# Kernel optimization log

Hardware: AMD Instinct MI355X
Metric: run time of the kernel (lower is better)

## Reference

```python
import jax, jax.numpy as jnp
import numpy as np

S, B, NC = 16, 8, 5
D, H, DH = 256, 16, 16
PS, IMG = 7, 28
P = (IMG // PS) ** 2  # 16 patches
L = 2
PD = PS * PS * 1  # 49
EF, EFT = 4, 0.5
DFT = int(EFT * D)


def layernorm(x, g, b, eps=1e-5):
    m = x.mean(-1, keepdims=True)
    v = ((x - m) ** 2).mean(-1, keepdims=True)
    return (x - m) / jnp.sqrt(v + eps) * g + b


def patchify(x):
    # 's b c (h p1) (w p2) -> s b (h w) (p1 p2 c)'
    s, bb, c, hh, ww = x.shape
    h, w = hh // PS, ww // PS
    x = x.reshape(s, bb, c, h, PS, w, PS)
    x = x.transpose(0, 1, 3, 5, 4, 6, 2)
    return x.reshape(s, bb, h * w, PS * PS * c)


def srwm(x, Wy, Wq, Wk, wb, ln_g, ln_b):
    # Stateful self-referential weight matrix layer (Irie et al. 2022).
    # x: (S, Bn, h*dh); Wy/Wq/Wk: (h, dh, dh); wb: (h, 4, dh)
    s, bn, dim = x.shape
    h, dh = Wy.shape[0], Wy.shape[1]
    xs = x.reshape(s, bn, h, dh)
    bc = lambda W: jnp.broadcast_to(W[None], (bn,) + W.shape)

    def step(carry, xt):
        Wy, Wq, Wk, wb = carry
        y = jnp.einsum('bhij,bhj->bhi', Wy, xt)
        q = jnp.einsum('bhij,bhj->bhi', Wq, xt)
        k = jnp.einsum('bhij,bhj->bhi', Wk, xt)
        beta = jax.nn.sigmoid(jnp.einsum('bhcj,bhj->bhc', wb, xt))  # (Bn,h,4)
        qs = jax.nn.softmax(q, -1)
        ks = jax.nn.softmax(k, -1)
        # old values retrieved with k, target values generated with q
        vy_k = jnp.einsum('bhij,bhj->bhi', Wy, ks)
        vq_k = jnp.einsum('bhij,bhj->bhi', Wq, ks)
        vk_k = jnp.einsum('bhij,bhj->bhi', Wk, ks)
        vb_k = jnp.einsum('bhcj,bhj->bhc', wb, ks)
        vy_q = jax.nn.softmax(jnp.einsum('bhij,bhj->bhi', Wy, qs), -1)
        vq_q = jnp.einsum('bhij,bhj->bhi', Wq, qs)
        vk_q = jnp.einsum('bhij,bhj->bhi', Wk, qs)
        vb_q = jnp.einsum('bhcj,bhj->bhc', wb, qs)
        upd = lambda d, bt: bt[..., None, None] * d[..., None] * ks[..., None, :]
        Wy = Wy + upd(vy_q - vy_k, beta[..., 0])
        Wq = Wq + upd(vq_q - vq_k, beta[..., 1])
        Wk = Wk + upd(vk_q - vk_k, beta[..., 2])
        wb = wb + beta[..., 3, None, None] * (vb_q - vb_k)[..., None] * ks[..., None, :]
        return (Wy, Wq, Wk, wb), y

    _, ys = jax.lax.scan(step, (bc(Wy), bc(Wq), bc(Wk), bc(wb)), xs)
    return layernorm(ys.reshape(s, bn, dim), ln_g, ln_b)


def setup_inputs():
    key = jax.random.key(0)
    ks = iter(jax.random.split(key, 64))
    n = lambda shape, sc: jax.random.normal(next(ks), shape, jnp.float32) * sc
    return dict(
        x=jax.random.normal(next(ks), (S, B, 1, IMG, IMG), jnp.float32),
        fb=jax.random.randint(next(ks), (S, B), 0, NC),
        in_W=n((PD + NC, D), (PD + NC) ** -0.5), in_b=jnp.zeros((D,)),
        tk_Wy=n((L, 1, P, P), P ** -0.5), tk_Wq=n((L, 1, P, P), 0.01 * P ** -0.5),
        tk_Wk=n((L, 1, P, P), P ** -0.5), tk_wb=n((L, 1, 4, P), P ** -0.5),
        tk_lng=jnp.ones((L, P)), tk_lnb=jnp.zeros((L, P)),
        tkm_g=jnp.ones((L, D)), tkm_b=jnp.zeros((L, D)),
        tkm_W1=n((L, P, EF * P), P ** -0.5), tkm_b1=jnp.zeros((L, EF * P)),
        tkm_W2=n((L, EF * P, P), (EF * P) ** -0.5), tkm_b2=jnp.zeros((L, P)),
        ch_Wy=n((L, H, DH, DH), DH ** -0.5), ch_Wq=n((L, H, DH, DH), 0.01 * DH ** -0.5),
        ch_Wk=n((L, H, DH, DH), DH ** -0.5), ch_wb=n((L, H, 4, DH), DH ** -0.5),
        ch_lng=jnp.ones((L, D)), ch_lnb=jnp.zeros((L, D)),
        chm_g=jnp.ones((L, D)), chm_b=jnp.zeros((L, D)),
        chm_W1=n((L, D, DFT), D ** -0.5), chm_b1=jnp.zeros((L, DFT)),
        chm_W2=n((L, DFT, D), DFT ** -0.5), chm_b2=jnp.zeros((L, D)),
        fln_g=jnp.ones((D,)), fln_b=jnp.zeros((D,)),
        o_Wy=n((H, DH, DH), DH ** -0.5), o_Wq=n((H, DH, DH), 0.01 * DH ** -0.5),
        o_Wk=n((H, DH, DH), DH ** -0.5), o_wb=n((H, 4, DH), DH ** -0.5),
        o_lng=jnp.ones((D,)), o_lnb=jnp.zeros((D,)),
        out_W=n((D, NC), D ** -0.5), out_b=jnp.zeros((NC,)),
    )


def reference(x, fb, in_W, in_b, tk_Wy, tk_Wq, tk_Wk, tk_wb, tk_lng, tk_lnb,
              tkm_g, tkm_b, tkm_W1, tkm_b1, tkm_W2, tkm_b2,
              ch_Wy, ch_Wq, ch_Wk, ch_wb, ch_lng, ch_lnb,
              chm_g, chm_b, chm_W1, chm_b1, chm_W2, chm_b2,
              fln_g, fln_b, o_Wy, o_Wq, o_Wk, o_wb, o_lng, o_lnb, out_W, out_b):
    xp = patchify(x)  # (S,B,P,PD)
    emb = jnp.broadcast_to(jax.nn.one_hot(fb, NC)[:, :, None, :], (S, B, P, NC))
    h = jnp.concatenate([xp, emb.astype(xp.dtype)], -1) @ in_W + in_b  # (S,B,P,D)
    for i in range(L):
        # token SRWM: features = patch axis, batch = B*D
        t = jnp.swapaxes(h, -2, -1).reshape(S, B * D, P)
        t = srwm(t, tk_Wy[i], tk_Wq[i], tk_Wk[i], tk_wb[i], tk_lng[i], tk_lnb[i])
        h = jnp.swapaxes(t.reshape(S, B, D, P), -2, -1)
        # token mixer (pre-norm residual, FFN over patch axis)
        hn = jnp.swapaxes(layernorm(h, tkm_g[i], tkm_b[i]), -2, -1)
        hn = jax.nn.gelu(hn @ tkm_W1[i] + tkm_b1[i]) @ tkm_W2[i] + tkm_b2[i]
        h = h + jnp.swapaxes(hn, -2, -1)
        # channel SRWM: features = hidden axis, batch = B*P
        c = srwm(h.reshape(S, B * P, D), ch_Wy[i], ch_Wq[i], ch_Wk[i], ch_wb[i], ch_lng[i], ch_lnb[i])
        h = c.reshape(S, B, P, D)
        # channel mixer
        hn = layernorm(h, chm_g[i], chm_b[i])
        h = h + (jax.nn.gelu(hn @ chm_W1[i] + chm_b1[i]) @ chm_W2[i] + chm_b2[i])
    h = layernorm(h, fln_g, fln_b).mean(-2)  # (S,B,D) mean over patches
    h = srwm(h, o_Wy, o_Wq, o_Wk, o_wb, o_lng, o_lnb)
    return h @ out_W + out_b  # (S,B,NC)
```

## Files before the change

### kernel.cpp

```cpp
#include <hip/hip_runtime.h>
#include <math.h>

constexpr int cS  = 16;
constexpr int cB  = 8;
constexpr int cNC = 5;
constexpr int cD  = 256;
constexpr int cP  = 16;
constexpr int cPD = 49;
#define LEPS 1e-5f

__device__ __forceinline__ float frcp(float x) { return __builtin_amdgcn_rcpf(x); }
__device__ __forceinline__ float sigm(float x) { return frcp(1.0f + __expf(-x)); }
__device__ __forceinline__ float gelu_t(float x) {
  const float z = 1.5957691216057308f * (x + 0.044715f * x * x * x);
  return x * frcp(1.0f + __expf(-z));
}

template<int CTRL>
__device__ __forceinline__ float dpp_mov(float v) {
  return __int_as_float(__builtin_amdgcn_update_dpp(
      0, __float_as_int(v), CTRL, 0xF, 0xF, true));
}
__device__ __forceinline__ float row_sum16(float v) {
  v += dpp_mov<0xB1>(v);
  v += dpp_mov<0x4E>(v);
  v += dpp_mov<0x124>(v);
  v += dpp_mov<0x128>(v);
  return v;
}
__device__ __forceinline__ float wave_sum64(float v) {
  v = row_sum16(v);
  v += __shfl_xor(v, 16, 64);
  v += __shfl_xor(v, 32, 64);
  return v;
}

__device__ __forceinline__ float srwm_step(
    float xv, float (&wy)[16], float (&wq)[16], float (&wk)[16], float (&wbr)[16]) {
  float y = 0.f, q = 0.f, k = 0.f, bt = 0.f;
#pragma unroll
  for (int j = 0; j < 16; ++j) {
    const float xj = __shfl(xv, j, 16);
    y += wy[j] * xj; q += wq[j] * xj; k += wk[j] * xj; bt += wbr[j] * xj;
  }
  const float bsig = sigm(bt);
  const float eq = __expf(q), ek = __expf(k);
  float ay = 0.f, vyk = 0.f, vqq = 0.f, vqk = 0.f, vkq = 0.f, vkk = 0.f, vbq = 0.f, vbk = 0.f;
  float ksj[16];
#pragma unroll
  for (int j = 0; j < 16; ++j) {
    const float qj = __shfl(eq, j, 16);
    const float kj = __shfl(ek, j, 16);
    ksj[j] = kj;
    ay  += wy[j]  * qj; vyk += wy[j]  * kj;
    vqq += wq[j]  * qj; vqk += wq[j]  * kj;
    vkq += wk[j]  * qj; vkk += wk[j]  * kj;
    vbq += wbr[j] * qj; vbk += wbr[j] * kj;
  }
  const float rq = frcp(row_sum16(eq));
  const float rk = frcp(row_sum16(ek));
  const float ea = __expf(ay * rq);
  const float vyq = ea * frcp(row_sum16(ea));
  const float b0  = __shfl(bsig, 0, 16);
  const float b1v = __shfl(bsig, 1, 16);
  const float b2v = __shfl(bsig, 2, 16);
  const float b3v = __shfl(bsig, 3, 16);
  const float cy = b0  * (vyq      - vyk * rk) * rk;
  const float cq = b1v * (vqq * rq - vqk * rk) * rk;
  const float ck = b2v * (vkq * rq - vkk * rk) * rk;
  const float cb = b3v * (vbq * rq - vbk * rk) * rk;
#pragma unroll
  for (int j = 0; j < 16; ++j) {
    wy[j] += cy * ksj[j]; wq[j] += cq * ksj[j]; wk[j] += ck * ksj[j]; wbr[j] += cb * ksj[j];
  }
  return y;
}

__global__ __launch_bounds__(256) void k_embed(const float* __restrict__ x,
                                               const int* __restrict__ fb,
                                               const float* __restrict__ inW,
                                               const float* __restrict__ inb,
                                               float* __restrict__ h) {
  const int blk = blockIdx.x;
  const int p  = blk & 15;
  const int sb = blk >> 4;
  const int ph = p >> 2, pw = p & 3;
  __shared__ float sx[cPD];
  const int t = threadIdx.x;
  if (t < cPD) {
    const int p1 = t / 7, p2 = t % 7;
    sx[t] = x[(size_t)sb * 784 + (ph * 7 + p1) * 28 + (pw * 7 + p2)];
  }
  __syncthreads();
  const int cls = fb[sb];
  float acc = inb[t] + inW[(size_t)(cPD + cls) * cD + t];
#pragma unroll
  for (int j = 0; j < cPD; ++j) acc += sx[j] * inW[(size_t)j * cD + t];
  h[((size_t)sb * cP + p) * cD + t] = acc;
}

__global__ __launch_bounds__(128) void k_tok_srwm(
    float* __restrict__ h, const float* __restrict__ Wy0, const float* __restrict__ Wq0,
    const float* __restrict__ Wk0, const float* __restrict__ wb0,
    const float* __restrict__ lng, const float* __restrict__ lnb) {
  const int t    = threadIdx.x;
  const int lane = t & 63;
  const int w    = t >> 6;
  const int r    = lane & 15;
  const int li   = lane >> 4;
  const int b    = blockIdx.x >> 5;
  const int d    = ((blockIdx.x & 31) << 3) + (w << 2) + li;
  float wy[16], wq[16], wk[16], wbr[16];
#pragma unroll
  for (int j = 0; j < 16; ++j) {
    wy[j]  = Wy0[r * 16 + j];
    wq[j]  = Wq0[r * 16 + j];
    wk[j]  = Wk0[r * 16 + j];
    wbr[j] = wb0[(r & 3) * 16 + j];
  }
  const float gg = lng[r], bb = lnb[r];
  float xp[16];
#pragma unroll
  for (int s = 0; s < 16; ++s)
    xp[s] = h[((size_t)(s * cB + b) * cP + r) * cD + d];
  for (int s = 0; s < cS; ++s) {
    const float y = srwm_step(xp[s], wy, wq, wk, wbr);
    const float s1 = row_sum16(y);
    const float s2 = row_sum16(y * y);
    const float m = s1 * 0.0625f;
    const float var = s2 * 0.0625f - m * m;
    h[((size_t)(s * cB + b) * cP + r) * cD + d] = (y - m) * rsqrtf(var + LEPS) * gg + bb;
  }
}

__global__ __launch_bounds__(256) void k_tok_mixer(
    float* __restrict__ h, const float* __restrict__ g, const float* __restrict__ bta,
    const float* __restrict__ W1, const float* __restrict__ b1,
    const float* __restrict__ W2, const float* __restrict__ b2) {
  const int sb = blockIdx.x;
  const int t = threadIdx.x;
  __shared__ float tile[16][256];
  __shared__ float W1s[16 * 64], W2s[64 * 16];
  __shared__ float mean_[16], rstd_[16];
  __shared__ float red[16][17], red2[16][17];
  const size_t base = (size_t)sb * cP * cD;
#pragma unroll
  for (int p = 0; p < 16; ++p) tile[p][t] = h[base + p * 256 + t];
  W1s[t] = W1[t]; W1s[t + 256] = W1[t + 256]; W1s[t + 512] = W1[t + 512]; W1s[t + 768] = W1[t + 768];
  W2s[t] = W2[t]; W2s[t + 256] = W2[t + 256]; W2s[t + 512] = W2[t + 512]; W2s[t + 768] = W2[t + 768];
  __syncthreads();
  const int p = t >> 4, l = t & 15;
  float ps = 0.f, ps2 = 0.f;
#pragma unroll
  for (int k = 0; k < 16; ++k) { const float v = tile[p][l + 16 * k]; ps += v; ps2 += v * v; }
  red[p][l] = ps; red2[p][l] = ps2;
  __syncthreads();
  if (t < 16) {
    float sm = 0.f, s2 = 0.f;
#pragma unroll
    for (int k = 0; k < 16; ++k) { sm += red[t][k]; s2 += red2[t][k]; }
    const float m = sm * (1.f / 256.f);
    mean_[t] = m;
    rstd_[t] = rsqrtf(s2 * (1.f / 256.f) - m * m + LEPS);
  }
  __syncthreads();
  const float gd = g[t], bd = bta[t];
  float v[16], out[16];
#pragma unroll
  for (int pp = 0; pp < 16; ++pp) {
    v[pp] = (tile[pp][t] - mean_[pp]) * rstd_[pp] * gd + bd;
    out[pp] = b2[pp];
  }
  for (int e = 0; e < 64; ++e) {
    float acc = b1[e];
#pragma unroll
    for (int pp = 0; pp < 16; ++pp) acc += v[pp] * W1s[pp * 64 + e];
    const float ge = gelu_t(acc);
#pragma unroll
    for (int pp = 0; pp < 16; ++pp) out[pp] += ge * W2s[e * 16 + pp];
  }
#pragma unroll
  for (int pp = 0; pp < 16; ++pp) h[base + pp * 256 + t] = tile[pp][t] + out[pp];
}

__global__ __launch_bounds__(128) void k_ch_scan(
    const float* __restrict__ h, float* __restrict__ y2,
    const float* __restrict__ Wy0, const float* __restrict__ Wq0,
    const float* __restrict__ Wk0, const float* __restrict__ wb0) {
  const int t  = threadIdx.x;
  const int hg = blockIdx.x & 1;
  const int bp = blockIdx.x >> 1;
  const int hh = (hg << 3) + (t >> 4);
  const int r  = t & 15;
  const int d  = (hg << 7) + t;
  float wy[16], wq[16], wk[16], wbr[16];
#pragma unroll
  for (int j = 0; j < 16; ++j) {
    wy[j]  = Wy0[(hh * 16 + r) * 16 + j];
    wq[j]  = Wq0[(hh * 16 + r) * 16 + j];
    wk[j]  = Wk0[(hh * 16 + r) * 16 + j];
    wbr[j] = wb0[(hh * 4 + (r & 3)) * 16 + j];
  }
  float xp[16];
#pragma unroll
  for (int s = 0; s < 16; ++s)
    xp[s] = h[(size_t)(s * cB * cP + bp) * cD + d];
  for (int s = 0; s < cS; ++s)
    y2[(size_t)(s * cB * cP + bp) * cD + d] = srwm_step(xp[s], wy, wq, wk, wbr);
}

__global__ __launch_bounds__(256) void k_ch_ln_mix(
    const float* __restrict__ y2, float* __restrict__ h,
    const float* __restrict__ lng, const float* __restrict__ lnb,
    const float* __restrict__ mg, const float* __restrict__ mb,
    const float* __restrict__ W1, const float* __restrict__ b1,
    const float* __restrict__ W2, const float* __restrict__ b2) {
  const int t = threadIdx.x;
  const int row0 = blockIdx.x * 8;
  __shared__ float yv[8][256];
  __shared__ float lnv[8][256];
  __shared__ float hid[8][128];
  const float4* yp4 = (const float4*)(y2 + (size_t)row0 * cD);
  ((float4*)yv)[t]       = yp4[t];
  ((float4*)yv)[t + 256] = yp4[t + 256];
  __syncthreads();
  const int r32 = t >> 5, l = t & 31;
  const float4 eg0 = ((const float4*)lng)[l * 2];
  const float4 eg1 = ((const float4*)lng)[l * 2 + 1];
  const float4 eb0 = ((const float4*)lnb)[l * 2];
  const float4 eb1 = ((const float4*)lnb)[l * 2 + 1];
  const float4 mg0 = ((const float4*)mg)[l * 2];
  const float4 mg1 = ((const float4*)mg)[l * 2 + 1];
  const float4 mb0 = ((const float4*)mb)[l * 2];
  const float4 mb1 = ((const float4*)mb)[l * 2 + 1];
  const float4 y0 = ((const float4*)yv[r32])[l * 2];
  const float4 y1 = ((const float4*)yv[r32])[l * 2 + 1];
  float s1 = y0.x + y0.y + y0.z + y0.w + y1.x + y1.y + y1.z + y1.w;
  float s2 = y0.x * y0.x + y0.y * y0.y + y0.z * y0.z + y0.w * y0.w +
             y1.x * y1.x + y1.y * y1.y + y1.z * y1.z + y1.w * y1.w;
#pragma unroll
  for (int o = 1; o < 32; o <<= 1) {
    s1 += __shfl_xor(s1, o, 32);
    s2 += __shfl_xor(s2, o, 32);
  }
  const float m1 = s1 * (1.f / 256.f);
  const float rst1 = rsqrtf(s2 * (1.f / 256.f) - m1 * m1 + LEPS);
  float4 a0, a1;
  a0.x = (y0.x - m1) * rst1 * eg0.x + eb0.x; a0.y = (y0.y - m1) * rst1 * eg0.y + eb0.y;
  a0.z = (y0.z - m1) * rst1 * eg0.z + eb0.z; a0.w = (y0.w - m1) * rst1 * eg0.w + eb0.w;
  a1.x = (y1.x - m1) * rst1 * eg1.x + eb1.x; a1.y = (y1.y - m1) * rst1 * eg1.y + eb1.y;
  a1.z = (y1.z - m1) * rst1 * eg1.z + eb1.z; a1.w = (y1.w - m1) * rst1 * eg1.w + eb1.w;
  float u1 = a0.x + a0.y + a0.z + a0.w + a1.x + a1.y + a1.z + a1.w;
  float u2 = a0.x * a0.x + a0.y * a0.y + a0.z * a0.z + a0.w * a0.w +
             a1.x * a1.x + a1.y * a1.y + a1.z * a1.z + a1.w * a1.w;
#pragma unroll
  for (int o = 1; o < 32; o <<= 1) {
    u1 += __shfl_xor(u1, o, 32);
    u2 += __shfl_xor(u2, o, 32);
  }
  const float m2 = u1 * (1.f / 256.f);
  const float rst2 = rsqrtf(u2 * (1.f / 256.f) - m2 * m2 + LEPS);
  float4 L0, L1;
  L0.x = (a0.x - m2) * rst2 * mg0.x + mb0.x; L0.y = (a0.y - m2) * rst2 * mg0.y + mb0.y;
  L0.z = (a0.z - m2) * rst2 * mg0.z + mb0.z; L0.w = (a0.w - m2) * rst2 * mg0.w + mb0.w;
  L1.x = (a1.x - m2) * rst2 * mg1.x + mb1.x; L1.y = (a1.y - m2) * rst2 * mg1.y + mb1.y;
  L1.z = (a1.z - m2) * rst2 * mg1.z + mb1.z; L1.w = (a1.w - m2) * rst2 * mg1.w + mb1.w;
  ((float4*)lnv[r32])[l * 2]     = L0;
  ((float4*)lnv[r32])[l * 2 + 1] = L1;
  __syncthreads();
  {
    const float4* W1f = (const float4*)W1;
    float4 acc = ((const float4*)b1)[l];
    for (int j = 0; j < 256; ++j) {
      const float xj = lnv[r32][j];
      const float4 wv = W1f[j * 32 + l];
      acc.x += xj * wv.x; acc.y += xj * wv.y; acc.z += xj * wv.z; acc.w += xj * wv.w;
    }
    float4 hv;
    hv.x = gelu_t(acc.x); hv.y = gelu_t(acc.y);
    hv.z = gelu_t(acc.z); hv.w = gelu_t(acc.w);
    ((float4*)hid[r32])[l] = hv;
  }
  __syncthreads();
  {
    const float4* W2f = (const float4*)W2;
    float4 o0 = ((const float4*)b2)[l * 2];
    float4 o1 = ((const float4*)b2)[l * 2 + 1];
    for (int e = 0; e < 128; ++e) {
      const float xh = hid[r32][e];
      const float4 w0 = W2f[e * 64 + l * 2];
      const float4 w1 = W2f[e * 64 + l * 2 + 1];
      o0.x += xh * w0.x; o0.y += xh * w0.y; o0.z += xh * w0.z; o0.w += xh * w0.w;
      o1.x += xh * w1.x; o1.y += xh * w1.y; o1.z += xh * w1.z; o1.w += xh * w1.w;
    }
    o0.x += a0.x; o0.y += a0.y; o0.z += a0.z; o0.w += a0.w;
    o1.x += a1.x; o1.y += a1.y; o1.z += a1.z; o1.w += a1.w;
    float4* op = (float4*)(h + ((size_t)row0 + r32) * cD);
    op[l * 2]     = o0;
    op[l * 2 + 1] = o1;
  }
}

__global__ __launch_bounds__(256) void k_fln_mean(
    const float* __restrict__ h, const float* __restrict__ gg, const float* __restrict__ bbv,
    float* __restrict__ o) {
  const int sb = blockIdx.x;
  const int t = threadIdx.x;
  const int lane = t & 63, w = t >> 6;
  const float4 g4 = ((const float4*)gg)[lane];
  const float4 b4 = ((const float4*)bbv)[lane];
  float a0 = 0.f, a1 = 0.f, a2 = 0.f, a3 = 0.f;
  for (int pp = 0; pp < 4; ++pp) {
    const int p = w * 4 + pp;
    const float4 v4 = ((const float4*)(h + ((size_t)sb * cP + p) * cD))[lane];
    const float s1 = wave_sum64(v4.x + v4.y + v4.z + v4.w);
    const float s2 = wave_sum64(v4.x * v4.x + v4.y * v4.y + v4.z * v4.z + v4.w * v4.w);
    const float m = s1 * (1.f / 256.f);
    const float rst = rsqrtf(s2 * (1.f / 256.f) - m * m + LEPS);
    a0 += (v4.x - m) * rst * g4.x + b4.x;
    a1 += (v4.y - m) * rst * g4.y + b4.y;
    a2 += (v4.z - m) * rst * g4.z + b4.z;
    a3 += (v4.w - m) * rst * g4.w + b4.w;
  }
  __shared__ float sacc[4][256];
  float4* sp = (float4*)sacc[w];
  sp[lane] = make_float4(a0, a1, a2, a3);
  __syncthreads();
  o[(size_t)sb * cD + t] = (sacc[0][t] + sacc[1][t] + sacc[2][t] + sacc[3][t]) * (1.f / 16.f);
}

__global__ __launch_bounds__(256, 1) void k_out_srwm(
    const float* __restrict__ gin, float* __restrict__ outp,
    const float* __restrict__ Wy0, const float* __restrict__ Wq0,
    const float* __restrict__ Wk0, const float* __restrict__ wb0,
    const float* __restrict__ lng, const float* __restrict__ lnb,
    const float* __restrict__ outW, const float* __restrict__ outb) {
  const int t = threadIdx.x;
  const int lane = t & 63;
  const int w = t >> 6;
  const int hh = t >> 4, r = t & 15;
  const int b = blockIdx.x;
  __shared__ float ymat[16][256];
  __shared__ float gwm[cNC][256];
  __shared__ float GBp[4][10];
  __shared__ float GBs[10];
  float wy[16], wq[16], wk[16], wbr[16];
#pragma unroll
  for (int j = 0; j < 16; ++j) {
    wy[j]  = Wy0[(hh * 16 + r) * 16 + j];
    wq[j]  = Wq0[(hh * 16 + r) * 16 + j];
    wk[j]  = Wk0[(hh * 16 + r) * 16 + j];
    wbr[j] = wb0[(hh * 4 + (r & 3)) * 16 + j];
  }
  {
    const float gg = lng[t], bbl = lnb[t];
    float pg[cNC], pbv[cNC];
#pragma unroll
    for (int c = 0; c < cNC; ++c) {
      const float wv = outW[(size_t)t * cNC + c];
      const float gwv = gg * wv;
      gwm[c][t] = gwv;
      pg[c] = wave_sum64(gwv);
      pbv[c] = wave_sum64(bbl * wv);
    }
    if (lane == 0) {
#pragma unroll
      for (int c = 0; c < cNC; ++c) { GBp[w][c] = pg[c]; GBp[w][5 + c] = pbv[c]; }
    }
    __syncthreads();
    if (t < 10) GBs[t] = GBp[0][t] + GBp[1][t] + GBp[2][t] + GBp[3][t];
    __syncthreads();
  }
  float xp[16];
#pragma unroll
  for (int s = 0; s < 16; ++s) xp[s] = gin[(size_t)(s * cB + b) * cD + t];
  for (int s = 0; s < cS; ++s)
    ymat[s][t] = srwm_step(xp[s], wy, wq, wk, wbr);
  __syncthreads();
  for (int k2 = 0; k2 < 4; ++k2) {
    const int sidx = w * 4 + k2;
    const float4 y4 = ((const float4*)ymat[sidx])[lane];
    const float s1 = wave_sum64(y4.x + y4.y + y4.z + y4.w);
    const float s2 = wave_sum64(y4.x * y4.x + y4.y * y4.y + y4.z * y4.z + y4.w * y4.w);
    float S[cNC];
#pragma unroll
    for (int c = 0; c < cNC; ++c) {
      const float4 g4 = ((const float4*)gwm[c])[lane];
      S[c] = wave_sum64(y4.x * g4.x + y4.y * g4.y + y4.z * g4.z + y4.w * g4.w);
    }
    if (lane == 0) {
      const float m = s1 * (1.f / 256.f);
      const float var = s2 * (1.f / 256.f) - m * m;
      const float rst = rsqrtf(var + LEPS);
#pragma unroll
      for (int c = 0; c < cNC; ++c) {
        outp[(size_t)(sidx * cB + b) * cNC + c] =
            outb[c] + rst * S[c] - rst * m * GBs[c] + GBs[5 + c];
      }
    }
  }
}

extern "C" void kernel_launch(void* const* d_in, const int* in_sizes, int n_in,
                              void* d_out, int out_size, void* d_ws, size_t ws_size,
                              hipStream_t stream) {
  const float* x     = (const float*)d_in[0];
  const int*   fb    = (const int*)d_in[1];
  const float* inW   = (const float*)d_in[2];
  const float* inb   = (const float*)d_in[3];
  const float* tkWy  = (const float*)d_in[4];
  const float* tkWq  = (const float*)d_in[5];
  const float* tkWk  = (const float*)d_in[6];
  const float* tkwb  = (const float*)d_in[7];
  const float* tklng = (const float*)d_in[8];
  const float* tklnb = (const float*)d_in[9];
  const float* tkmg  = (const float*)d_in[10];
  const float* tkmb  = (const float*)d_in[11];
  const float* tkmW1 = (const float*)d_in[12];
  const float* tkmb1 = (const float*)d_in[13];
  const float* tkmW2 = (const float*)d_in[14];
  const float* tkmb2 = (const float*)d_in[15];
  const float* chWy  = (const float*)d_in[16];
  const float* chWq  = (const float*)d_in[17];
  const float* chWk  = (const float*)d_in[18];
  const float* chwb  = (const float*)d_in[19];
  const float* chlng = (const float*)d_in[20];
  const float* chlnb = (const float*)d_in[21];
  const float* chmg  = (const float*)d_in[22];
  const float* chmb  = (const float*)d_in[23];
  const float* chmW1 = (const float*)d_in[24];
  const float* chmb1 = (const float*)d_in[25];
  const float* chmW2 = (const float*)d_in[26];
  const float* chmb2 = (const float*)d_in[27];
  const float* flng  = (const float*)d_in[28];
  const float* flnb  = (const float*)d_in[29];
  const float* oWy   = (const float*)d_in[30];
  const float* oWq   = (const float*)d_in[31];
  const float* oWk   = (const float*)d_in[32];
  const float* owb   = (const float*)d_in[33];
  const float* olng  = (const float*)d_in[34];
  const float* olnb  = (const float*)d_in[35];
  const float* outW  = (const float*)d_in[36];
  const float* outb  = (const float*)d_in[37];

  float* h    = (float*)d_ws;
  float* gbuf = h + (size_t)cS * cB * cP * cD;
  float* y2   = gbuf + (size_t)cS * cB * cD;
  float* outp = (float*)d_out;

  k_embed<<<dim3(cS * cB * cP), dim3(256), 0, stream>>>(x, fb, inW, inb, h);
  for (int i = 0; i < 2; ++i) {
    k_tok_srwm<<<dim3(256), dim3(128), 0, stream>>>(
        h, tkWy + i * 256, tkWq + i * 256, tkWk + i * 256, tkwb + i * 64,
        tklng + i * 16, tklnb + i * 16);
    k_tok_mixer<<<dim3(cS * cB), dim3(256), 0, stream>>>(
        h, tkmg + i * 256, tkmb + i * 256, tkmW1 + i * 1024, tkmb1 + i * 64,
        tkmW2 + i * 1024, tkmb2 + i * 16);
    k_ch_scan<<<dim3(cB * cP * 2), dim3(128), 0, stream>>>(
        h, y2, chWy + i * 4096, chWq + i * 4096, chWk + i * 4096, chwb + i * 1024);
    k_ch_ln_mix<<<dim3(cS * cB * cP / 8), dim3(256), 0, stream>>>(
        y2, h, chlng + i * 256, chlnb + i * 256,
        chmg + i * 256, chmb + i * 256, chmW1 + i * 32768, chmb1 + i * 128,
        chmW2 + i * 32768, chmb2 + i * 256);
  }
  k_fln_mean<<<dim3(cS * cB), dim3(256), 0, stream>>>(h, flng, flnb, gbuf);
  k_out_srwm<<<dim3(cB), dim3(256), 0, stream>>>(
      gbuf, outp, oWy, oWq, oWk, owb, olng, olnb, outW, outb);
}
```

Baseline: 313.9 us.

## Fuse patch embedding into token SRWM and final LayerNorm-mean into channel mixer

Removes the standalone embedding kernel. The first token-SRWM launch now loads the 16 images for its batch into shared memory (about 50 KB) and computes the patch projection directly into registers. It also removes the final LayerNorm+mean kernel: in the last layer the channel LN/mixer kernel processes all 16 patches of one (s,b) per block and writes the pooled result directly. This saves two launches and the round trips of h through global memory. The cost is a large shared buffer in the SRWM kernel that may limit occupancy, and only 128 blocks for the last mixer instead of 256.

```diff
diff --git a/kernel.cpp b/kernel.cpp
--- a/kernel.cpp
+++ b/kernel.cpp
@@ -76,33 +76,12 @@
   return y;
 }
 
-__global__ __launch_bounds__(256) void k_embed(const float* __restrict__ x,
-                                               const int* __restrict__ fb,
-                                               const float* __restrict__ inW,
-                                               const float* __restrict__ inb,
-                                               float* __restrict__ h) {
-  const int blk = blockIdx.x;
-  const int p  = blk & 15;
-  const int sb = blk >> 4;
-  const int ph = p >> 2, pw = p & 3;
-  __shared__ float sx[cPD];
-  const int t = threadIdx.x;
-  if (t < cPD) {
-    const int p1 = t / 7, p2 = t % 7;
-    sx[t] = x[(size_t)sb * 784 + (ph * 7 + p1) * 28 + (pw * 7 + p2)];
-  }
-  __syncthreads();
-  const int cls = fb[sb];
-  float acc = inb[t] + inW[(size_t)(cPD + cls) * cD + t];
-#pragma unroll
-  for (int j = 0; j < cPD; ++j) acc += sx[j] * inW[(size_t)j * cD + t];
-  h[((size_t)sb * cP + p) * cD + t] = acc;
-}
-
-__global__ __launch_bounds__(128) void k_tok_srwm(
+__global__ __launch_bounds__(128, 1) void k_tok_srwm(
     float* __restrict__ h, const float* __restrict__ Wy0, const float* __restrict__ Wq0,
     const float* __restrict__ Wk0, const float* __restrict__ wb0,
-    const float* __restrict__ lng, const float* __restrict__ lnb) {
+    const float* __restrict__ lng, const float* __restrict__ lnb,
+    int we, const float* __restrict__ x, const int* __restrict__ fb,
+    const float* __restrict__ inW, const float* __restrict__ inb) {
   const int t    = threadIdx.x;
   const int lane = t & 63;
   const int w    = t >> 6;
@@ -110,6 +89,7 @@
   const int li   = lane >> 4;
   const int b    = blockIdx.x >> 5;
   const int d    = ((blockIdx.x & 31) << 3) + (w << 2) + li;
+  __shared__ float img[cS * 784];
   float wy[16], wq[16], wk[16], wbr[16];
 #pragma unroll
   for (int j = 0; j < 16; ++j) {
@@ -120,9 +100,31 @@
   }
   const float gg = lng[r], bb = lnb[r];
   float xp[16];
-#pragma unroll
-  for (int s = 0; s < 16; ++s)
-    xp[s] = h[((size_t)(s * cB + b) * cP + r) * cD + d];
+  if (we) {
+    for (int idx = t; idx < cS * 784; idx += 128) {
+      const int s = idx / 784, pix = idx % 784;
+      img[idx] = x[(size_t)(s * cB + b) * 784 + pix];
+    }
+    float winreg[cPD];
+#pragma unroll
+    for (int j = 0; j < cPD; ++j) winreg[j] = inW[(size_t)j * cD + d];
+    const float ib = inb[d];
+    const int pixbase = (r >> 2) * 196 + (r & 3) * 7;
+    __syncthreads();
+#pragma unroll
+    for (int s = 0; s < cS; ++s) {
+      const int cls = fb[s * cB + b];
+      float acc = ib + inW[(size_t)(cPD + cls) * cD + d];
+#pragma unroll
+      for (int j = 0; j < cPD; ++j)
+        acc += img[s * 784 + pixbase + (j / 7) * 28 + (j % 7)] * winreg[j];
+      xp[s] = acc;
+    }
+  } else {
+#pragma unroll
+    for (int s = 0; s < 16; ++s)
+      xp[s] = h[((size_t)(s * cB + b) * cP + r) * cD + d];
+  }
   for (int s = 0; s < cS; ++s) {
     const float y = srwm_step(xp[s], wy, wq, wk, wbr);
     const float s1 = row_sum16(y);
@@ -209,21 +211,22 @@
     y2[(size_t)(s * cB * cP + bp) * cD + d] = srwm_step(xp[s], wy, wq, wk, wbr);
 }
 
+template<int DOFLN>
 __global__ __launch_bounds__(256) void k_ch_ln_mix(
     const float* __restrict__ y2, float* __restrict__ h,
     const float* __restrict__ lng, const float* __restrict__ lnb,
     const float* __restrict__ mg, const float* __restrict__ mb,
     const float* __restrict__ W1, const float* __restrict__ b1,
-    const float* __restrict__ W2, const float* __restrict__ b2) {
+    const float* __restrict__ W2, const float* __restrict__ b2,
+    const float* __restrict__ flng, const float* __restrict__ flnb,
+    float* __restrict__ gbuf) {
   const int t = threadIdx.x;
-  const int row0 = blockIdx.x * 8;
+  const int row0 = blockIdx.x * (DOFLN ? 16 : 8);
   __shared__ float yv[8][256];
   __shared__ float lnv[8][256];
   __shared__ float hid[8][128];
-  const float4* yp4 = (const float4*)(y2 + (size_t)row0 * cD);
-  ((float4*)yv)[t]       = yp4[t];
-  ((float4*)yv)[t + 256] = yp4[t + 256];
-  __syncthreads();
+  __shared__ float hstore[DOFLN ? 16 : 1][256];
+  __shared__ float mean_[16], rstd_[16];
   const int r32 = t >> 5, l = t & 31;
   const float4 eg0 = ((const float4*)lng)[l * 2];
   const float4 eg1 = ((const float4*)lng)[l * 2 + 1];
@@ -233,100 +236,110 @@
   const float4 mg1 = ((const float4*)mg)[l * 2 + 1];
   const float4 mb0 = ((const float4*)mb)[l * 2];
   const float4 mb1 = ((const float4*)mb)[l * 2 + 1];
-  const float4 y0 = ((const float4*)yv[r32])[l * 2];
-  const float4 y1 = ((const float4*)yv[r32])[l * 2 + 1];
-  float s1 = y0.x + y0.y + y0.z + y0.w + y1.x + y1.y + y1.z + y1.w;
-  float s2 = y0.x * y0.x + y0.y * y0.y + y0.z * y0.z + y0.w * y0.w +
-             y1.x * y1.x + y1.y * y1.y + y1.z * y1.z + y1.w * y1.w;
-#pragma unroll
-  for (int o = 1; o < 32; o <<= 1) {
-    s1 += __shfl_xor(s1, o, 32);
-    s2 += __shfl_xor(s2, o, 32);
-  }
-  const float m1 = s1 * (1.f / 256.f);
-  const float rst1 = rsqrtf(s2 * (1.f / 256.f) - m1 * m1 + LEPS);
-  float4 a0, a1;
-  a0.x = (y0.x - m1) * rst1 * eg0.x + eb0.x; a0.y = (y0.y - m1) * rst1 * eg0.y + eb0.y;
-  a0.z = (y0.z - m1) * rst1 * eg0.z + eb0.z; a0.w = (y0.w - m1) * rst1 * eg0.w + eb0.w;
-  a1.x = (y1.x - m1) * rst1 * eg1.x + eb1.x; a1.y = (y1.y - m1) * rst1 * eg1.y + eb1.y;
-  a1.z = (y1.z - m1) * rst1 * eg1.z + eb1.z; a1.w = (y1.w - m1) * rst1 * eg1.w + eb1.w;
-  float u1 = a0.x + a0.y + a0.z + a0.w + a1.x + a1.y + a1.z + a1.w;
-  float u2 = a0.x * a0.x + a0.y * a0.y + a0.z * a0.z + a0.w * a0.w +
-             a1.x * a1.x + a1.y * a1.y + a1.z * a1.z + a1.w * a1.w;
-#pragma unroll
-  for (int o = 1; o < 32; o <<= 1) {
-    u1 += __shfl_xor(u1, o, 32);
-    u2 += __shfl_xor(u2, o, 32);
-  }
-  const float m2 = u1 * (1.f / 256.f);
-  const float rst2 = rsqrtf(u2 * (1.f / 256.f) - m2 * m2 + LEPS);
-  float4 L0, L1;
-  L0.x = (a0.x - m2) * rst2 * mg0.x + mb0.x; L0.y = (a0.y - m2) * rst2 * mg0.y + mb0.y;
-  L0.z = (a0.z - m2) * rst2 * mg0.z + mb0.z; L0.w = (a0.w - m2) * rst2 * mg0.w + mb0.w;
-  L1.x = (a1.x - m2) * rst2 * mg1.x + mb1.x; L1.y = (a1.y - m2) * rst2 * mg1.y + mb1.y;
-  L1.z = (a1.z - m2) * rst2 * mg1.z + mb1.z; L1.w = (a1.w - m2) * rst2 * mg1.w + mb1.w;
-  ((float4*)lnv[r32])[l * 2]     = L0;
-  ((float4*)lnv[r32])[l * 2 + 1] = L1;
-  __syncthreads();
-  {
-    const float4* W1f = (const float4*)W1;
-    float4 acc = ((const float4*)b1)[l];
-    for (int j = 0; j < 256; ++j) {
-      const float xj = lnv[r32][j];
-      const float4 wv = W1f[j * 32 + l];
-      acc.x += xj * wv.x; acc.y += xj * wv.y; acc.z += xj * wv.z; acc.w += xj * wv.w;
-    }
-    float4 hv;
-    hv.x = gelu_t(acc.x); hv.y = gelu_t(acc.y);
-    hv.z = gelu_t(acc.z); hv.w = gelu_t(acc.w);
-    ((float4*)hid[r32])[l] = hv;
-  }
-  __syncthreads();
-  {
-    const float4* W2f = (const float4*)W2;
-    float4 o0 = ((const float4*)b2)[l * 2];
-    float4 o1 = ((const float4*)b2)[l * 2 + 1];
-    for (int e = 0; e < 128; ++e) {
-      const float xh = hid[r32][e];
-      const float4 w0 = W2f[e * 64 + l * 2];
-      const float4 w1 = W2f[e * 64 + l * 2 + 1];
-      o0.x += xh * w0.x; o0.y += xh * w0.y; o0.z += xh * w0.z; o0.w += xh * w0.w;
-      o1.x += xh * w1.x; o1.y += xh * w1.y; o1.z += xh * w1.z; o1.w += xh * w1.w;
-    }
-    o0.x += a0.x; o0.y += a0.y; o0.z += a0.z; o0.w += a0.w;
-    o1.x += a1.x; o1.y += a1.y; o1.z += a1.z; o1.w += a1.w;
-    float4* op = (float4*)(h + ((size_t)row0 + r32) * cD);
-    op[l * 2]     = o0;
-    op[l * 2 + 1] = o1;
-  }
-}
-
-__global__ __launch_bounds__(256) void k_fln_mean(
-    const float* __restrict__ h, const float* __restrict__ gg, const float* __restrict__ bbv,
-    float* __restrict__ o) {
-  const int sb = blockIdx.x;
-  const int t = threadIdx.x;
-  const int lane = t & 63, w = t >> 6;
-  const float4 g4 = ((const float4*)gg)[lane];
-  const float4 b4 = ((const float4*)bbv)[lane];
-  float a0 = 0.f, a1 = 0.f, a2 = 0.f, a3 = 0.f;
-  for (int pp = 0; pp < 4; ++pp) {
-    const int p = w * 4 + pp;
-    const float4 v4 = ((const float4*)(h + ((size_t)sb * cP + p) * cD))[lane];
-    const float s1 = wave_sum64(v4.x + v4.y + v4.z + v4.w);
-    const float s2 = wave_sum64(v4.x * v4.x + v4.y * v4.y + v4.z * v4.z + v4.w * v4.w);
-    const float m = s1 * (1.f / 256.f);
-    const float rst = rsqrtf(s2 * (1.f / 256.f) - m * m + LEPS);
-    a0 += (v4.x - m) * rst * g4.x + b4.x;
-    a1 += (v4.y - m) * rst * g4.y + b4.y;
-    a2 += (v4.z - m) * rst * g4.z + b4.z;
-    a3 += (v4.w - m) * rst * g4.w + b4.w;
-  }
-  __shared__ float sacc[4][256];
-  float4* sp = (float4*)sacc[w];
-  sp[lane] = make_float4(a0, a1, a2, a3);
-  __syncthreads();
-  o[(size_t)sb * cD + t] = (sacc[0][t] + sacc[1][t] + sacc[2][t] + sacc[3][t]) * (1.f / 16.f);
+  for (int grp = 0; grp < (DOFLN ? 2 : 1); ++grp) {
+    const int gr0 = row0 + grp * 8;
+    const float4* yp4 = (const float4*)(y2 + (size_t)gr0 * cD);
+    ((float4*)yv)[t]       = yp4[t];
+    ((float4*)yv)[t + 256] = yp4[t + 256];
+    __syncthreads();
+    const float4 y0 = ((const float4*)yv[r32])[l * 2];
+    const float4 y1 = ((const float4*)yv[r32])[l * 2 + 1];
+    float s1 = y0.x + y0.y + y0.z + y0.w + y1.x + y1.y + y1.z + y1.w;
+    float s2 = y0.x * y0.x + y0.y * y0.y + y0.z * y0.z + y0.w * y0.w +
+               y1.x * y1.x + y1.y * y1.y + y1.z * y1.z + y1.w * y1.w;
+#pragma unroll
+    for (int o = 1; o < 32; o <<= 1) {
+      s1 += __shfl_xor(s1, o, 32);
+      s2 += __shfl_xor(s2, o, 32);
+    }
+    const float m1 = s1 * (1.f / 256.f);
+    const float rst1 = rsqrtf(s2 * (1.f / 256.f) - m1 * m1 + LEPS);
+    float4 a0, a1;
+    a0.x = (y0.x - m1) * rst1 * eg0.x + eb0.x; a0.y = (y0.y - m1) * rst1 * eg0.y + eb0.y;
+    a0.z = (y0.z - m1) * rst1 * eg0.z + eb0.z; a0.w = (y0.w - m1) * rst1 * eg0.w + eb0.w;
+    a1.x = (y1.x - m1) * rst1 * eg1.x + eb1.x; a1.y = (y1.y - m1) * rst1 * eg1.y + eb1.y;
+    a1.z = (y1.z - m1) * rst1 * eg1.z + eb1.z; a1.w = (y1.w - m1) * rst1 * eg1.w + eb1.w;
+    float u1 = a0.x + a0.y + a0.z + a0.w + a1.x + a1.y + a1.z + a1.w;
+    float u2 = a0.x * a0.x + a0.y * a0.y + a0.z * a0.z + a0.w * a0.w +
+               a1.x * a1.x + a1.y * a1.y + a1.z * a1.z + a1.w * a1.w;
+#pragma unroll
+    for (int o = 1; o < 32; o <<= 1) {
+      u1 += __shfl_xor(u1, o, 32);
+      u2 += __shfl_xor(u2, o, 32);
+    }
+    const float m2 = u1 * (1.f / 256.f);
+    const float rst2 = rsqrtf(u2 * (1.f / 256.f) - m2 * m2 + LEPS);
+    float4 L0, L1;
+    L0.x = (a0.x - m2) * rst2 * mg0.x + mb0.x; L0.y = (a0.y - m2) * rst2 * mg0.y + mb0.y;
+    L0.z = (a0.z - m2) * rst2 * mg0.z + mb0.z; L0.w = (a0.w - m2) * rst2 * mg0.w + mb0.w;
+    L1.x = (a1.x - m2) * rst2 * mg1.x + mb1.x; L1.y = (a1.y - m2) * rst2 * mg1.y + mb1.y;
+    L1.z = (a1.z - m2) * rst2 * mg1.z + mb1.z; L1.w = (a1.w - m2) * rst2 * mg1.w + mb1.w;
+    ((float4*)lnv[r32])[l * 2]     = L0;
+    ((float4*)lnv[r32])[l * 2 + 1] = L1;
+    __syncthreads();
+    {
+      const float4* W1f = (const float4*)W1;
+      float4 acc = ((const float4*)b1)[l];
+      for (int j = 0; j < 256; ++j) {
+        const float xj = lnv[r32][j];
+        const float4 wv = W1f[j * 32 + l];
+        acc.x += xj * wv.x; acc.y += xj * wv.y; acc.z += xj * wv.z; acc.w += xj * wv.w;
+      }
+      float4 hv;
+      hv.x = gelu_t(acc.x); hv.y = gelu_t(acc.y);
+      hv.z = gelu_t(acc.z); hv.w = gelu_t(acc.w);
+      ((float4*)hid[r32])[l] = hv;
+    }
+    __syncthreads();
+    {
+      const float4* W2f = (const float4*)W2;
+      float4 o0 = ((const float4*)b2)[l * 2];
+      float4 o1 = ((const float4*)b2)[l * 2 + 1];
+      for (int e = 0; e < 128; ++e) {
+        const float xh = hid[r32][e];
+        const float4 w0 = W2f[e * 64 + l * 2];
+        const float4 w1 = W2f[e * 64 + l * 2 + 1];
+        o0.x += xh * w0.x; o0.y += xh * w0.y; o0.z += xh * w0.z; o0.w += xh * w0.w;
+        o1.x += xh * w1.x; o1.y += xh * w1.y; o1.z += xh * w1.z; o1.w += xh * w1.w;
+      }
+      o0.x += a0.x; o0.y += a0.y; o0.z += a0.z; o0.w += a0.w;
+      o1.x += a1.x; o1.y += a1.y; o1.z += a1.z; o1.w += a1.w;
+      if constexpr (DOFLN) {
+        ((float4*)hstore[grp * 8 + r32])[l * 2]     = o0;
+        ((float4*)hstore[grp * 8 + r32])[l * 2 + 1] = o1;
+      } else {
+        float4* op = (float4*)(h + ((size_t)gr0 + r32) * cD);
+        op[l * 2]     = o0;
+        op[l * 2 + 1] = o1;
+      }
+    }
+    __syncthreads();
+  }
+  if constexpr (DOFLN) {
+    for (int rr = r32; rr < 16; rr += 8) {
+      const float4 v0 = ((const float4*)hstore[rr])[l * 2];
+      const float4 v1 = ((const float4*)hstore[rr])[l * 2 + 1];
+      float s1 = v0.x + v0.y + v0.z + v0.w + v1.x + v1.y + v1.z + v1.w;
+      float s2 = v0.x * v0.x + v0.y * v0.y + v0.z * v0.z + v0.w * v0.w +
+                 v1.x * v1.x + v1.y * v1.y + v1.z * v1.z + v1.w * v1.w;
+#pragma unroll
+      for (int o = 1; o < 32; o <<= 1) {
+        s1 += __shfl_xor(s1, o, 32);
+        s2 += __shfl_xor(s2, o, 32);
+      }
+      if (l == 0) {
+        const float m = s1 * (1.f / 256.f);
+        mean_[rr] = m;
+        rstd_[rr] = rsqrtf(s2 * (1.f / 256.f) - m * m + LEPS);
+      }
+    }
+    __syncthreads();
+    float acc = 0.f;
+#pragma unroll
+    for (int p = 0; p < 16; ++p)
+      acc += (hstore[p][t] - mean_[p]) * rstd_[p];
+    gbuf[(size_t)blockIdx.x * cD + t] = flng[t] * acc * (1.f / 16.f) + flnb[t];
+  }
 }
 
 __global__ __launch_bounds__(256, 1) void k_out_srwm(
@@ -448,22 +461,28 @@
   float* y2   = gbuf + (size_t)cS * cB * cD;
   float* outp = (float*)d_out;
 
-  k_embed<<<dim3(cS * cB * cP), dim3(256), 0, stream>>>(x, fb, inW, inb, h);
   for (int i = 0; i < 2; ++i) {
     k_tok_srwm<<<dim3(256), dim3(128), 0, stream>>>(
         h, tkWy + i * 256, tkWq + i * 256, tkWk + i * 256, tkwb + i * 64,
-        tklng + i * 16, tklnb + i * 16);
+        tklng + i * 16, tklnb + i * 16,
+        (i == 0) ? 1 : 0, x, fb, inW, inb);
     k_tok_mixer<<<dim3(cS * cB), dim3(256), 0, stream>>>(
         h, tkmg + i * 256, tkmb + i * 256, tkmW1 + i * 1024, tkmb1 + i * 64,
         tkmW2 + i * 1024, tkmb2 + i * 16);
     k_ch_scan<<<dim3(cB * cP * 2), dim3(128), 0, stream>>>(
         h, y2, chWy + i * 4096, chWq + i * 4096, chWk + i * 4096, chwb + i * 1024);
-    k_ch_ln_mix<<<dim3(cS * cB * cP / 8), dim3(256), 0, stream>>>(
-        y2, h, chlng + i * 256, chlnb + i * 256,
-        chmg + i * 256, chmb + i * 256, chmW1 + i * 32768, chmb1 + i * 128,
-        chmW2 + i * 32768, chmb2 + i * 256);
-  }
-  k_fln_mean<<<dim3(cS * cB), dim3(256), 0, stream>>>(h, flng, flnb, gbuf);
+    if (i == 0) {
+      k_ch_ln_mix<0><<<dim3(cS * cB * cP / 8), dim3(256), 0, stream>>>(
+          y2, h, chlng + i * 256, chlnb + i * 256,
+          chmg + i * 256, chmb + i * 256, chmW1 + i * 32768, chmb1 + i * 128,
+          chmW2 + i * 32768, chmb2 + i * 256, flng, flnb, gbuf);
+    } else {
+      k_ch_ln_mix<1><<<dim3(cS * cB), dim3(256), 0, stream>>>(
+          y2, h, chlng + i * 256, chlnb + i * 256,
+          chmg + i * 256, chmb + i * 256, chmW1 + i * 32768, chmb1 + i * 128,
+          chmW2 + i * 32768, chmb2 + i * 256, flng, flnb, gbuf);
+    }
+  }
   k_out_srwm<<<dim3(cB), dim3(256), 0, stream>>>(
       gbuf, outp, oWy, oWq, oWk, owb, olng, olnb, outW, outb);
 }
```

New measurement: 346.4 us. 10.3% more time.
